# Optimization experiments

Hardware: AMD Instinct MI355X
Metric: run time of the kernel (lower is better)

Reference implementation:

```python
import jax, jax.numpy as jnp
import numpy as np

SEQ_LEN, BZ, D_IN = 512, 64, 1024
HIDDEN, D_OUT, NUM_LANG = 256, 1024, 16


def setup_inputs() -> dict:
    key = jax.random.key(0)
    ks = jax.random.split(key, 6)
    x = jax.random.normal(ks[0], (SEQ_LEN, BZ, D_IN), dtype=jnp.float32)
    lang_ids = jax.random.randint(ks[1], (BZ,), 0, NUM_LANG, dtype=jnp.int64)
    # Per-language 2-layer MLP params, stacked over the language axis.
    # Stored as [in, out] so y = x @ W + b (same math as torch Linear's x @ W.T + b).
    s1 = 1.0 / np.sqrt(D_IN)
    s2 = 1.0 / np.sqrt(HIDDEN)
    W1 = jax.random.uniform(ks[2], (NUM_LANG, D_IN, HIDDEN), jnp.float32, -s1, s1)
    b1 = jax.random.uniform(ks[3], (NUM_LANG, HIDDEN), jnp.float32, -s1, s1)
    W2 = jax.random.uniform(ks[4], (NUM_LANG, HIDDEN, D_OUT), jnp.float32, -s2, s2)
    b2 = jax.random.uniform(ks[5], (NUM_LANG, D_OUT), jnp.float32, -s2, s2)
    return {"x": x, "lang_ids": lang_ids, "W1": W1, "b1": b1, "W2": W2, "b2": b2}


def reference(x, lang_ids, W1, b1, W2, b2):
    # Gather each batch element's expert weights, then do batched GEMMs.
    # Equivalent to the torch loop (dispatch -> per-expert MLP -> combine),
    # without redundant gather/scatter passes.
    W1g = W1[lang_ids]            # [bz, d_in, hidden]
    b1g = b1[lang_ids]            # [bz, hidden]
    W2g = W2[lang_ids]            # [bz, hidden, d_out]
    b2g = b2[lang_ids]            # [bz, d_out]
    h = jnp.einsum('sbd,bdh->sbh', x, W1g) + b1g[None, :, :]
    h = jax.nn.relu(h)
    y = jnp.einsum('sbh,bho->sbo', h, W2g) + b2g[None, :, :]
    return y
```

## Files before the change

kernel.cpp:

```cpp
#include <hip/hip_runtime.h>

#define SEQ 512
#define BZ  64
#define DIN 1024
#define HID 256
#define DOUT 1024
#define NLANG 16

typedef __attribute__((ext_vector_type(8))) __bf16 bf16x8;
typedef __attribute__((ext_vector_type(4))) float f32x4;

__device__ __forceinline__ unsigned int f2bf_pack(float lo, float hi) {
    unsigned short a = __builtin_bit_cast(unsigned short, (__bf16)lo);
    unsigned short b = __builtin_bit_cast(unsigned short, (__bf16)hi);
    return (unsigned int)a | ((unsigned int)b << 16);
}

__global__ __launch_bounds__(256)
void transpose_cvt(const float* __restrict__ src, unsigned short* __restrict__ dst,
                   int R, int C) {
    __shared__ float tile[64][65];
    const int l  = blockIdx.x;
    const int rb = blockIdx.y * 64;
    const int cb = blockIdx.z * 64;
    const float* s = src + (long)l * R * C;
    unsigned short* d = dst + (long)l * R * C;
    const int t = threadIdx.x;
#pragma unroll
    for (int j = 0; j < 4; ++j) {
        int u = t + 256 * j;
        int r = u >> 4, c4 = u & 15;
        float4 v = *(const float4*)(s + (long)(rb + r) * C + cb + c4 * 4);
        tile[r][c4 * 4 + 0] = v.x; tile[r][c4 * 4 + 1] = v.y;
        tile[r][c4 * 4 + 2] = v.z; tile[r][c4 * 4 + 3] = v.w;
    }
    __syncthreads();
#pragma unroll
    for (int j = 0; j < 4; ++j) {
        int u = t + 256 * j;
        int dr = u >> 4, dc4 = u & 15;
        uint2 o;
        o.x = f2bf_pack(tile[dc4 * 4 + 0][dr], tile[dc4 * 4 + 1][dr]);
        o.y = f2bf_pack(tile[dc4 * 4 + 2][dr], tile[dc4 * 4 + 3][dr]);
        *(uint2*)(d + (long)(cb + dr) * R + rb + dc4 * 4) = o;
    }
}

template<int KTOT, int NTOT, bool AF32, bool L1RELU>
__global__ __launch_bounds__(256)
void mlp_gemm(const void* __restrict__ Ap,
              const unsigned short* __restrict__ Wt,
              const float* __restrict__ bias,
              const int* __restrict__ lang,
              void* __restrict__ outp) {
    __shared__ uint4 sAq[64 * 64 * 2 / 16];
    __shared__ uint4 sWq[256 * 64 * 2 / 16];
    char* sA = (char*)sAq;
    char* sW = (char*)sWq;

    const int b    = blockIdx.x;
    const int st   = blockIdx.y;
    const int nblk = blockIdx.z;
    const int t    = threadIdx.x;
    const int lane = t & 63;
    const int w    = t >> 6;
    const int lid  = lang[b];
    const int s0   = st * 64;

    const float*          Af = (const float*)Ap;
    const unsigned short* Ah = (const unsigned short*)Ap;
    const long Abase = (long)s0 * BZ * KTOT + (long)b * KTOT;
    const unsigned short* Wbase = Wt + ((long)lid * NTOT + (long)nblk * 256) * KTOT;

    const f32x4 zero4 = {0.f, 0.f, 0.f, 0.f};
    f32x4 acc[4][4];
#pragma unroll
    for (int mi = 0; mi < 4; ++mi)
#pragma unroll
        for (int ni = 0; ni < 4; ++ni) acc[mi][ni] = zero4;

    for (int kt = 0; kt < KTOT / 64; ++kt) {
        if constexpr (AF32) {
#pragma unroll
            for (int j = 0; j < 4; ++j) {
                int u = t + 256 * j;
                int m = u >> 4, c4 = u & 15;
                const float4 v = *(const float4*)(Af + Abase + (long)m * (BZ * KTOT) + kt * 64 + c4 * 4);
                uint2 p;
                p.x = f2bf_pack(v.x, v.y);
                p.y = f2bf_pack(v.z, v.w);
                *(uint2*)(sA + (((m * 128) + c4 * 8) ^ ((m & 7) << 4))) = p;
            }
        } else {
#pragma unroll
            for (int j = 0; j < 2; ++j) {
                int u = t + 256 * j;
                int m = u >> 3, c16 = u & 7;
                const uint4 v = *(const uint4*)(Ah + Abase + (long)m * (BZ * KTOT) + kt * 64 + c16 * 8);
                *(uint4*)(sA + (((m * 128) + c16 * 16) ^ ((m & 7) << 4))) = v;
            }
        }
#pragma unroll
        for (int j = 0; j < 8; ++j) {
            int u = t + 256 * j;
            int n = u >> 3, c16 = u & 7;
            const uint4 v = *(const uint4*)(Wbase + (long)n * KTOT + kt * 64 + c16 * 8);
            *(uint4*)(sW + (((n * 128) + c16 * 16) ^ ((n & 7) << 4))) = v;
        }
        __syncthreads();

#pragma unroll
        for (int ks = 0; ks < 2; ++ks) {
            const int kb = (ks * 32 + ((lane >> 4) * 8)) * 2;
            bf16x8 av[4], bv[4];
#pragma unroll
            for (int mi = 0; mi < 4; ++mi) {
                int r = mi * 16 + (lane & 15);
                av[mi] = __builtin_bit_cast(bf16x8,
                    *(const uint4*)(sA + ((r * 128 + kb) ^ ((r & 7) << 4))));
            }
#pragma unroll
            for (int ni = 0; ni < 4; ++ni) {
                int n = w * 64 + ni * 16 + (lane & 15);
                bv[ni] = __builtin_bit_cast(bf16x8,
                    *(const uint4*)(sW + ((n * 128 + kb) ^ ((n & 7) << 4))));
            }
#pragma unroll
            for (int mi = 0; mi < 4; ++mi)
#pragma unroll
                for (int ni = 0; ni < 4; ++ni)
                    acc[mi][ni] = __builtin_amdgcn_mfma_f32_16x16x32_bf16(
                        av[mi], bv[ni], acc[mi][ni], 0, 0, 0);
        }
        __syncthreads();
    }

    float bvv[4];
#pragma unroll
    for (int ni = 0; ni < 4; ++ni)
        bvv[ni] = bias[(long)lid * NTOT + nblk * 256 + w * 64 + ni * 16 + (lane & 15)];

#pragma unroll
    for (int mi = 0; mi < 4; ++mi) {
#pragma unroll
        for (int r = 0; r < 4; ++r) {
            const int  row = mi * 16 + (lane >> 4) * 4 + r;
            const long s   = s0 + row;
#pragma unroll
            for (int ni = 0; ni < 4; ++ni) {
                const int col = nblk * 256 + w * 64 + ni * 16 + (lane & 15);
                float v = acc[mi][ni][r] + bvv[ni];
                if constexpr (L1RELU) {
                    v = v > 0.f ? v : 0.f;
                    ((unsigned short*)outp)[(s * BZ + b) * NTOT + col] =
                        __builtin_bit_cast(unsigned short, (__bf16)v);
                } else {
                    ((float*)outp)[(s * BZ + b) * NTOT + col] = v;
                }
            }
        }
    }
}

extern "C" void kernel_launch(void* const* d_in, const int* in_sizes, int n_in,
                              void* d_out, int out_size, void* d_ws, size_t ws_size,
                              hipStream_t stream) {
    const float* x    = (const float*)d_in[0];
    const int*   lang = (const int*)d_in[1];
    const float* W1   = (const float*)d_in[2];
    const float* b1   = (const float*)d_in[3];
    const float* W2   = (const float*)d_in[4];
    const float* b2   = (const float*)d_in[5];
    float* y = (float*)d_out;

    const size_t w1t_bytes = (size_t)NLANG * HID * DIN * 2;
    const size_t w2t_bytes = (size_t)NLANG * DOUT * HID * 2;
    unsigned short* W1t = (unsigned short*)d_ws;
    unsigned short* W2t = (unsigned short*)((char*)d_ws + w1t_bytes);
    unsigned short* h   = (unsigned short*)((char*)d_ws + w1t_bytes + w2t_bytes);

    transpose_cvt<<<dim3(NLANG, DIN / 64, HID / 64), 256, 0, stream>>>(W1, W1t, DIN, HID);
    transpose_cvt<<<dim3(NLANG, HID / 64, DOUT / 64), 256, 0, stream>>>(W2, W2t, HID, DOUT);

    mlp_gemm<DIN, HID, true, true>
        <<<dim3(BZ, SEQ / 64, HID / 256), 256, 0, stream>>>(x, W1t, b1, lang, h);

    mlp_gemm<HID, DOUT, false, false>
        <<<dim3(BZ, SEQ / 64, DOUT / 256), 256, 0, stream>>>(h, W2t, b2, lang, y);
}
```

Baseline: 112.3 us.

## Fuse both MLP layers in one kernel with prepacked MFMA weight fragments

Replaces the two separate GEMM kernels with one fused kernel that keeps the 64x256 hidden activations in shared memory, so the bf16 intermediate h is never written to or read from global memory. Weights are pre-packed into MFMA-fragment order by a new prep kernel and then loaded straight from global into registers, with no LDS staging. x tiles are double-buffered through registers and LDS, and W2 fragments are software-prefetched. The cost is high register use and occupancy capped at two blocks per CU, with each block doing the full second-layer N range serially.

Measured after the change: 102.3 us. -8.9%, faster.

```diff
diff --git a/kernel.cpp b/kernel.cpp
--- a/kernel.cpp
+++ b/kernel.cpp
@@ -10,156 +10,214 @@
 typedef __attribute__((ext_vector_type(8))) __bf16 bf16x8;
 typedef __attribute__((ext_vector_type(4))) float f32x4;
 
+__device__ __forceinline__ unsigned short f2bf(float f) {
+    return __builtin_bit_cast(unsigned short, (__bf16)f);
+}
 __device__ __forceinline__ unsigned int f2bf_pack(float lo, float hi) {
-    unsigned short a = __builtin_bit_cast(unsigned short, (__bf16)lo);
-    unsigned short b = __builtin_bit_cast(unsigned short, (__bf16)hi);
-    return (unsigned int)a | ((unsigned int)b << 16);
-}
-
+    return (unsigned int)f2bf(lo) | ((unsigned int)f2bf(hi) << 16);
+}
+
+template<int K, int N>
 __global__ __launch_bounds__(256)
-void transpose_cvt(const float* __restrict__ src, unsigned short* __restrict__ dst,
-                   int R, int C) {
-    __shared__ float tile[64][65];
-    const int l  = blockIdx.x;
-    const int rb = blockIdx.y * 64;
-    const int cb = blockIdx.z * 64;
-    const float* s = src + (long)l * R * C;
-    unsigned short* d = dst + (long)l * R * C;
-    const int t = threadIdx.x;
-#pragma unroll
-    for (int j = 0; j < 4; ++j) {
-        int u = t + 256 * j;
-        int r = u >> 4, c4 = u & 15;
-        float4 v = *(const float4*)(s + (long)(rb + r) * C + cb + c4 * 4);
-        tile[r][c4 * 4 + 0] = v.x; tile[r][c4 * 4 + 1] = v.y;
-        tile[r][c4 * 4 + 2] = v.z; tile[r][c4 * 4 + 3] = v.w;
-    }
+void prep_frags(const float* __restrict__ src, unsigned short* __restrict__ dst) {
+    constexpr int K32 = K / 32, N16 = N / 16;
+    const int gid = blockIdx.x * 256 + threadIdx.x;
+    const int l   = gid & 63;
+    const int f   = gid >> 6;
+    const int k32 = f & (K32 - 1);
+    const int n16 = (f / K32) & (N16 - 1);
+    const int lid = f / (K32 * N16);
+    const float* s = src + ((long)lid * K + k32 * 32 + (l >> 4) * 8) * N + n16 * 16 + (l & 15);
+    unsigned short o[8];
+#pragma unroll
+    for (int j = 0; j < 8; ++j) o[j] = f2bf(s[(long)j * N]);
+    uint4 v;
+    v.x = (unsigned int)o[0] | ((unsigned int)o[1] << 16);
+    v.y = (unsigned int)o[2] | ((unsigned int)o[3] << 16);
+    v.z = (unsigned int)o[4] | ((unsigned int)o[5] << 16);
+    v.w = (unsigned int)o[6] | ((unsigned int)o[7] << 16);
+    *(uint4*)(dst + (long)gid * 8) = v;
+}
+
+__global__ __launch_bounds__(256, 2)
+void fused_mlp(const float* __restrict__ x,
+               const unsigned short* __restrict__ W1f,
+               const float* __restrict__ b1,
+               const unsigned short* __restrict__ W2f,
+               const float* __restrict__ b2,
+               const int* __restrict__ lang,
+               float* __restrict__ y) {
+    __shared__ unsigned short sA[2][64 * 64];
+    __shared__ unsigned short sH[64 * 256];
+
+    const int b  = blockIdx.x;
+    const int st = blockIdx.y;
+    const int t  = threadIdx.x;
+    const int l  = t & 63;
+    const int w  = t >> 6;
+    const int lid = lang[b];
+    const int s0  = st * 64;
+    const long xbase = (long)s0 * BZ * DIN + (long)b * DIN;
+
+    const f32x4 z4 = {0.f, 0.f, 0.f, 0.f};
+
+    f32x4 acc1[4][4];
+#pragma unroll
+    for (int mi = 0; mi < 4; ++mi)
+#pragma unroll
+        for (int ni = 0; ni < 4; ++ni) acc1[mi][ni] = z4;
+
+    float4 xr[4];
+#define LOADX(KT)                                                                 \
+    {                                                                             \
+        _Pragma("unroll")                                                         \
+        for (int j = 0; j < 4; ++j) {                                             \
+            int u = t + 256 * j, m = u >> 4, c4 = u & 15;                         \
+            xr[j] = *(const float4*)(x + xbase + (long)m * (BZ * DIN) + (KT) * 64 + c4 * 4); \
+        }                                                                         \
+    }
+#define WRITEX(BUF)                                                               \
+    {                                                                             \
+        char* cA = (char*)sA[BUF];                                                \
+        _Pragma("unroll")                                                         \
+        for (int j = 0; j < 4; ++j) {                                             \
+            int u = t + 256 * j, m = u >> 4, c4 = u & 15;                         \
+            uint2 p;                                                              \
+            p.x = f2bf_pack(xr[j].x, xr[j].y);                                    \
+            p.y = f2bf_pack(xr[j].z, xr[j].w);                                    \
+            *(uint2*)(cA + (((m * 128) + c4 * 8) ^ ((m & 7) << 4))) = p;          \
+        }                                                                         \
+    }
+
+    LOADX(0);
+    WRITEX(0);
     __syncthreads();
-#pragma unroll
-    for (int j = 0; j < 4; ++j) {
-        int u = t + 256 * j;
-        int dr = u >> 4, dc4 = u & 15;
-        uint2 o;
-        o.x = f2bf_pack(tile[dc4 * 4 + 0][dr], tile[dc4 * 4 + 1][dr]);
-        o.y = f2bf_pack(tile[dc4 * 4 + 2][dr], tile[dc4 * 4 + 3][dr]);
-        *(uint2*)(d + (long)(cb + dr) * R + rb + dc4 * 4) = o;
-    }
-}
-
-template<int KTOT, int NTOT, bool AF32, bool L1RELU>
-__global__ __launch_bounds__(256)
-void mlp_gemm(const void* __restrict__ Ap,
-              const unsigned short* __restrict__ Wt,
-              const float* __restrict__ bias,
-              const int* __restrict__ lang,
-              void* __restrict__ outp) {
-    __shared__ uint4 sAq[64 * 64 * 2 / 16];
-    __shared__ uint4 sWq[256 * 64 * 2 / 16];
-    char* sA = (char*)sAq;
-    char* sW = (char*)sWq;
-
-    const int b    = blockIdx.x;
-    const int st   = blockIdx.y;
-    const int nblk = blockIdx.z;
-    const int t    = threadIdx.x;
-    const int lane = t & 63;
-    const int w    = t >> 6;
-    const int lid  = lang[b];
-    const int s0   = st * 64;
-
-    const float*          Af = (const float*)Ap;
-    const unsigned short* Ah = (const unsigned short*)Ap;
-    const long Abase = (long)s0 * BZ * KTOT + (long)b * KTOT;
-    const unsigned short* Wbase = Wt + ((long)lid * NTOT + (long)nblk * 256) * KTOT;
-
-    const f32x4 zero4 = {0.f, 0.f, 0.f, 0.f};
-    f32x4 acc[4][4];
-#pragma unroll
-    for (int mi = 0; mi < 4; ++mi)
-#pragma unroll
-        for (int ni = 0; ni < 4; ++ni) acc[mi][ni] = zero4;
-
-    for (int kt = 0; kt < KTOT / 64; ++kt) {
-        if constexpr (AF32) {
-#pragma unroll
-            for (int j = 0; j < 4; ++j) {
-                int u = t + 256 * j;
-                int m = u >> 4, c4 = u & 15;
-                const float4 v = *(const float4*)(Af + Abase + (long)m * (BZ * KTOT) + kt * 64 + c4 * 4);
-                uint2 p;
-                p.x = f2bf_pack(v.x, v.y);
-                p.y = f2bf_pack(v.z, v.w);
-                *(uint2*)(sA + (((m * 128) + c4 * 8) ^ ((m & 7) << 4))) = p;
-            }
-        } else {
-#pragma unroll
-            for (int j = 0; j < 2; ++j) {
-                int u = t + 256 * j;
-                int m = u >> 3, c16 = u & 7;
-                const uint4 v = *(const uint4*)(Ah + Abase + (long)m * (BZ * KTOT) + kt * 64 + c16 * 8);
-                *(uint4*)(sA + (((m * 128) + c16 * 16) ^ ((m & 7) << 4))) = v;
-            }
+
+    const unsigned short* w1p = W1f + (((long)lid * 16 + w * 4) * 32) * 512 + (long)l * 8;
+
+    for (int kt = 0; kt < 16; ++kt) {
+        const int cur = kt & 1;
+        if (kt < 15) LOADX(kt + 1);
+
+        bf16x8 bv[2][4];
+#pragma unroll
+        for (int ks = 0; ks < 2; ++ks)
+#pragma unroll
+            for (int ni = 0; ni < 4; ++ni)
+                bv[ks][ni] = __builtin_bit_cast(bf16x8,
+                    *(const uint4*)(w1p + (long)ni * 16384 + (kt * 2 + ks) * 512));
+
+        char* cA = (char*)sA[cur];
+#pragma unroll
+        for (int ks = 0; ks < 2; ++ks) {
+            bf16x8 av[4];
+#pragma unroll
+            for (int mi = 0; mi < 4; ++mi) {
+                int row = mi * 16 + (l & 15);
+                int ch  = ks * 4 + (l >> 4);
+                av[mi] = __builtin_bit_cast(bf16x8,
+                    *(const uint4*)(cA + row * 128 + ((ch ^ (row & 7)) << 4)));
+            }
+#pragma unroll
+            for (int mi = 0; mi < 4; ++mi)
+#pragma unroll
+                for (int ni = 0; ni < 4; ++ni)
+                    acc1[mi][ni] = __builtin_amdgcn_mfma_f32_16x16x32_bf16(
+                        av[mi], bv[ks][ni], acc1[mi][ni], 0, 0, 0);
         }
-#pragma unroll
-        for (int j = 0; j < 8; ++j) {
-            int u = t + 256 * j;
-            int n = u >> 3, c16 = u & 7;
-            const uint4 v = *(const uint4*)(Wbase + (long)n * KTOT + kt * 64 + c16 * 8);
-            *(uint4*)(sW + (((n * 128) + c16 * 16) ^ ((n & 7) << 4))) = v;
-        }
+
+        if (kt < 15) WRITEX(cur ^ 1);
         __syncthreads();
-
-#pragma unroll
-        for (int ks = 0; ks < 2; ++ks) {
-            const int kb = (ks * 32 + ((lane >> 4) * 8)) * 2;
-            bf16x8 av[4], bv[4];
-#pragma unroll
-            for (int mi = 0; mi < 4; ++mi) {
-                int r = mi * 16 + (lane & 15);
-                av[mi] = __builtin_bit_cast(bf16x8,
-                    *(const uint4*)(sA + ((r * 128 + kb) ^ ((r & 7) << 4))));
-            }
-#pragma unroll
-            for (int ni = 0; ni < 4; ++ni) {
-                int n = w * 64 + ni * 16 + (lane & 15);
-                bv[ni] = __builtin_bit_cast(bf16x8,
-                    *(const uint4*)(sW + ((n * 128 + kb) ^ ((n & 7) << 4))));
+    }
+
+    {
+        float bvv[4];
+#pragma unroll
+        for (int ni = 0; ni < 4; ++ni)
+            bvv[ni] = b1[lid * HID + w * 64 + ni * 16 + (l & 15)];
+        char* cH = (char*)sH;
+#pragma unroll
+        for (int mi = 0; mi < 4; ++mi)
+#pragma unroll
+            for (int r = 0; r < 4; ++r) {
+                int row = mi * 16 + (l >> 4) * 4 + r;
+#pragma unroll
+                for (int ni = 0; ni < 4; ++ni) {
+                    int col = w * 64 + ni * 16 + (l & 15);
+                    float v = acc1[mi][ni][r] + bvv[ni];
+                    v = v > 0.f ? v : 0.f;
+                    *(unsigned short*)(cH + row * 512 + (((col >> 3) ^ (row & 7)) << 4)
+                                       + (col & 7) * 2) = f2bf(v);
+                }
+            }
+    }
+    __syncthreads();
+
+    bf16x8 a2[4][8];
+    {
+        char* cH = (char*)sH;
+#pragma unroll
+        for (int mi = 0; mi < 4; ++mi)
+#pragma unroll
+            for (int ks = 0; ks < 8; ++ks) {
+                int row = mi * 16 + (l & 15);
+                int ch  = ks * 4 + (l >> 4);
+                a2[mi][ks] = __builtin_bit_cast(bf16x8,
+                    *(const uint4*)(cH + row * 512 + ((ch ^ (row & 7)) << 4)));
+            }
+    }
+
+    const unsigned short* w2p = W2f + (((long)lid * 64 + w * 16) * 8) * 512 + (long)l * 8;
+
+#pragma unroll 1
+    for (int nc = 0; nc < 4; ++nc) {
+        f32x4 acc[4][4];
+#pragma unroll
+        for (int mi = 0; mi < 4; ++mi)
+#pragma unroll
+            for (int ni = 0; ni < 4; ++ni) acc[mi][ni] = z4;
+
+        const unsigned short* wp = w2p + (long)nc * 4 * 4096;
+
+        bf16x8 pv[2][4];
+#pragma unroll
+        for (int ni = 0; ni < 4; ++ni)
+            pv[0][ni] = __builtin_bit_cast(bf16x8, *(const uint4*)(wp + (long)ni * 4096));
+#pragma unroll
+        for (int ks = 0; ks < 8; ++ks) {
+            const int cb = ks & 1;
+            if (ks < 7) {
+#pragma unroll
+                for (int ni = 0; ni < 4; ++ni)
+                    pv[cb ^ 1][ni] = __builtin_bit_cast(bf16x8,
+                        *(const uint4*)(wp + (long)ni * 4096 + (ks + 1) * 512));
             }
 #pragma unroll
             for (int mi = 0; mi < 4; ++mi)
 #pragma unroll
                 for (int ni = 0; ni < 4; ++ni)
                     acc[mi][ni] = __builtin_amdgcn_mfma_f32_16x16x32_bf16(
-                        av[mi], bv[ni], acc[mi][ni], 0, 0, 0);
+                        a2[mi][ks], pv[cb][ni], acc[mi][ni], 0, 0, 0);
         }
-        __syncthreads();
-    }
-
-    float bvv[4];
-#pragma unroll
-    for (int ni = 0; ni < 4; ++ni)
-        bvv[ni] = bias[(long)lid * NTOT + nblk * 256 + w * 64 + ni * 16 + (lane & 15)];
-
-#pragma unroll
-    for (int mi = 0; mi < 4; ++mi) {
-#pragma unroll
-        for (int r = 0; r < 4; ++r) {
-            const int  row = mi * 16 + (lane >> 4) * 4 + r;
-            const long s   = s0 + row;
-#pragma unroll
-            for (int ni = 0; ni < 4; ++ni) {
-                const int col = nblk * 256 + w * 64 + ni * 16 + (lane & 15);
-                float v = acc[mi][ni][r] + bvv[ni];
-                if constexpr (L1RELU) {
-                    v = v > 0.f ? v : 0.f;
-                    ((unsigned short*)outp)[(s * BZ + b) * NTOT + col] =
-                        __builtin_bit_cast(unsigned short, (__bf16)v);
-                } else {
-                    ((float*)outp)[(s * BZ + b) * NTOT + col] = v;
+
+        float b2v[4];
+#pragma unroll
+        for (int ni = 0; ni < 4; ++ni)
+            b2v[ni] = b2[lid * DOUT + w * 256 + nc * 64 + ni * 16 + (l & 15)];
+#pragma unroll
+        for (int mi = 0; mi < 4; ++mi)
+#pragma unroll
+            for (int r = 0; r < 4; ++r) {
+                int row = mi * 16 + (l >> 4) * 4 + r;
+#pragma unroll
+                for (int ni = 0; ni < 4; ++ni) {
+                    int col = w * 256 + nc * 64 + ni * 16 + (l & 15);
+                    y[((long)(s0 + row) * BZ + b) * DOUT + col] = acc[mi][ni][r] + b2v[ni];
                 }
             }
-        }
-    }
+    }
+#undef LOADX
+#undef WRITEX
 }
 
 extern "C" void kernel_launch(void* const* d_in, const int* in_sizes, int n_in,
@@ -173,18 +231,11 @@
     const float* b2   = (const float*)d_in[5];
     float* y = (float*)d_out;
 
-    const size_t w1t_bytes = (size_t)NLANG * HID * DIN * 2;
-    const size_t w2t_bytes = (size_t)NLANG * DOUT * HID * 2;
-    unsigned short* W1t = (unsigned short*)d_ws;
-    unsigned short* W2t = (unsigned short*)((char*)d_ws + w1t_bytes);
-    unsigned short* h   = (unsigned short*)((char*)d_ws + w1t_bytes + w2t_bytes);
-
-    transpose_cvt<<<dim3(NLANG, DIN / 64, HID / 64), 256, 0, stream>>>(W1, W1t, DIN, HID);
-    transpose_cvt<<<dim3(NLANG, HID / 64, DOUT / 64), 256, 0, stream>>>(W2, W2t, HID, DOUT);
-
-    mlp_gemm<DIN, HID, true, true>
-        <<<dim3(BZ, SEQ / 64, HID / 256), 256, 0, stream>>>(x, W1t, b1, lang, h);
-
-    mlp_gemm<HID, DOUT, false, false>
-        <<<dim3(BZ, SEQ / 64, DOUT / 256), 256, 0, stream>>>(h, W2t, b2, lang, y);
-}
+    unsigned short* W1f = (unsigned short*)d_ws;
+    unsigned short* W2f = (unsigned short*)((char*)d_ws + (size_t)NLANG * HID * DIN * 2);
+
+    prep_frags<DIN, HID><<<2048, 256, 0, stream>>>(W1, W1f);
+    prep_frags<HID, DOUT><<<2048, 256, 0, stream>>>(W2, W2f);
+
+    fused_mlp<<<dim3(BZ, SEQ / 64), 256, 0, stream>>>(x, W1f, b1, W2f, b2, lang, y);
+}
```
